# Kernel tuning notes

Hardware: AMD Instinct MI355X
Metric: run time of the kernel (lower is better)

Reference implementation:

```python
import jax, jax.numpy as jnp
import numpy as np

D_MODEL = 1024
NHEAD = 16
HEAD_DIM = D_MODEL // NHEAD
LN_EPS = 1e-5


def _layer_norm(x, g, b):
    mu = jnp.mean(x, axis=-1, keepdims=True)
    var = jnp.var(x, axis=-1, keepdims=True)
    return (x - mu) * jax.lax.rsqrt(var + LN_EPS) * g + b


def setup_inputs() -> dict:
    key = jax.random.key(0)
    ks = jax.random.split(key, 12)
    B, S = 2, 2048
    init = 0.02
    return {
        "query": jax.random.normal(ks[0], (B, S, D_MODEL), jnp.float32),
        "key_": jax.random.normal(ks[1], (B, S, D_MODEL), jnp.float32),
        "value": jax.random.normal(ks[2], (B, S, D_MODEL), jnp.float32),
        "Wq": jax.random.normal(ks[3], (D_MODEL, D_MODEL), jnp.float32) * init,
        "bq": jnp.zeros((D_MODEL,), jnp.float32),
        "Wk": jax.random.normal(ks[4], (D_MODEL, D_MODEL), jnp.float32) * init,
        "bk": jnp.zeros((D_MODEL,), jnp.float32),
        "Wv": jax.random.normal(ks[5], (D_MODEL, D_MODEL), jnp.float32) * init,
        "bv": jnp.zeros((D_MODEL,), jnp.float32),
        "Wo": jax.random.normal(ks[6], (D_MODEL, D_MODEL), jnp.float32) * init,
        "bo": jnp.zeros((D_MODEL,), jnp.float32),
        "ln_g": jnp.ones((D_MODEL,), jnp.float32),
        "ln_b": jnp.zeros((D_MODEL,), jnp.float32),
    }


def reference(query, key_, value, Wq, bq, Wk, bk, Wv, bv, Wo, bo, ln_g, ln_b):
    B, T, D = query.shape
    S = key_.shape[1]
    # shared LayerNorm applied to q, k, v inputs (as in the torch module)
    qn = _layer_norm(query, ln_g, ln_b)
    kn = _layer_norm(key_, ln_g, ln_b)
    vn = _layer_norm(value, ln_g, ln_b)
    # projections (torch Linear: x @ W.T + b)
    q = qn @ Wq.T + bq
    k = kn @ Wk.T + bk
    v = vn @ Wv.T + bv
    # [B, H, S, Dh]
    q = q.reshape(B, T, NHEAD, HEAD_DIM).transpose(0, 2, 1, 3)
    k = k.reshape(B, S, NHEAD, HEAD_DIM).transpose(0, 2, 1, 3)
    v = v.reshape(B, S, NHEAD, HEAD_DIM).transpose(0, 2, 1, 3)
    q = q * (HEAD_DIM ** -0.5)
    # [B, H, T, S] score matrix (explicitly materialized, as in source)
    scores = jnp.einsum("bhtd,bhsd->bhts", q, k)
    causal = jnp.triu(jnp.ones((T, S), dtype=bool), k=1)
    scores = jnp.where(causal, -jnp.inf, scores)
    attn = jax.nn.softmax(scores.astype(jnp.float32), axis=-1).astype(query.dtype)
    out = jnp.einsum("bhts,bhsd->bhtd", attn, v)
    out = out.transpose(0, 2, 1, 3).reshape(B, T, D)
    out = out @ Wo.T + bo
    return out, attn
```

## Files before the change

kernel.cpp:

```cpp
#include <hip/hip_runtime.h>
#include <hip/hip_bf16.h>

typedef unsigned short u16;
typedef unsigned int u32;
typedef __bf16 bf16x8 __attribute__((ext_vector_type(8)));
typedef float f32x4 __attribute__((ext_vector_type(4)));

__device__ __forceinline__ u16 f2bf(float f) {
  __hip_bfloat16 h = __float2bfloat16(f);
  u16 u;
  __builtin_memcpy(&u, &h, 2);
  return u;
}
__device__ __forceinline__ float bf2f(u16 u) {
  u32 b = ((u32)u) << 16;
  float f;
  __builtin_memcpy(&f, &b, 4);
  return f;
}

__device__ __forceinline__ void gload16(const u16* g, u16* l) {
  __builtin_amdgcn_global_load_lds(
      (const __attribute__((address_space(1))) u32*)g,
      (__attribute__((address_space(3))) u32*)l, 16, 0, 0);
}

__global__ __launch_bounds__(256) void ln_cast(
    const float* __restrict__ q, const float* __restrict__ k,
    const float* __restrict__ v, const float* __restrict__ g,
    const float* __restrict__ bb, u16* __restrict__ xn) {
  int row = blockIdx.x;
  int tsel = row >> 12;
  int r_in = row & 4095;
  const float* src = (tsel == 0) ? q : (tsel == 1) ? k : v;
  int tid = threadIdx.x;
  float4 x = ((const float4*)(src + (size_t)r_in * 1024))[tid];
  float s  = x.x + x.y + x.z + x.w;
  float ss = x.x * x.x + x.y * x.y + x.z * x.z + x.w * x.w;
  #pragma unroll
  for (int m = 1; m < 64; m <<= 1) { s += __shfl_xor(s, m); ss += __shfl_xor(ss, m); }
  __shared__ float red[8];
  int wid = tid >> 6;
  if ((tid & 63) == 0) { red[wid] = s; red[wid + 4] = ss; }
  __syncthreads();
  s  = red[0] + red[1] + red[2] + red[3];
  ss = red[4] + red[5] + red[6] + red[7];
  float mu  = s * (1.f / 1024.f);
  float var = ss * (1.f / 1024.f) - mu * mu;
  float rs  = rsqrtf(var + 1e-5f);
  float4 gv = ((const float4*)g)[tid];
  float4 bv = ((const float4*)bb)[tid];
  ushort4 o;
  o.x = f2bf((x.x - mu) * rs * gv.x + bv.x);
  o.y = f2bf((x.y - mu) * rs * gv.y + bv.y);
  o.z = f2bf((x.z - mu) * rs * gv.z + bv.z);
  o.w = f2bf((x.w - mu) * rs * gv.w + bv.w);
  ((ushort4*)(xn + (size_t)row * 1024))[tid] = o;
}

__global__ __launch_bounds__(256) void wcast(
    const float* __restrict__ wq, const float* __restrict__ wk,
    const float* __restrict__ wv, const float* __restrict__ wo,
    u16* __restrict__ dst) {
  int i = blockIdx.x * 256 + threadIdx.x;
  int e = i * 4;
  int sel = e >> 20;
  int loc = e & 1048575;
  const float* w = (sel == 0) ? wq : (sel == 1) ? wk : (sel == 2) ? wv : wo;
  float4 x = *(const float4*)(w + loc);
  ushort4 o;
  o.x = f2bf(x.x); o.y = f2bf(x.y); o.z = f2bf(x.z); o.w = f2bf(x.w);
  *(ushort4*)(dst + e) = o;
}

__global__ __launch_bounds__(256) void gemm_nt(
    const u16* __restrict__ A0, const u16* __restrict__ W0,
    const float* __restrict__ bias0, const float* __restrict__ bias1,
    const float* __restrict__ bias2,
    float* __restrict__ oF, u16* __restrict__ oP, u16* __restrict__ oVT,
    int mode) {
  __shared__ alignas(16) u16 Al[128][64];
  __shared__ alignas(16) u16 Bl[128][64];
  int z = blockIdx.z;
  const u16* A = A0 + (size_t)z * 4194304;
  const u16* W = W0 + (size_t)z * 1048576;
  const float* bias = (z == 0) ? bias0 : (z == 1) ? bias1 : bias2;
  int m0 = blockIdx.y * 128, n0 = blockIdx.x * 128;
  int tid = threadIdx.x;
  int lane = tid & 63, wid = tid >> 6;
  int wr = wid >> 1, wc = wid & 1;
  int l15 = lane & 15, lg = lane >> 4;
  int lr = lane >> 3, lc = lane & 7;

  f32x4 acc[4][4];
  #pragma unroll
  for (int i = 0; i < 4; ++i)
    #pragma unroll
    for (int j = 0; j < 4; ++j) acc[i][j] = (f32x4){0.f, 0.f, 0.f, 0.f};

  for (int kt = 0; kt < 1024; kt += 64) {
    __syncthreads();
    #pragma unroll
    for (int qq = 0; qq < 4; ++qq) {
      int rb = (qq * 4 + wid) * 8;
      gload16(A + (size_t)(m0 + rb + lr) * 1024 + kt + lc * 8, &Al[rb][0]);
      gload16(W + (size_t)(n0 + rb + lr) * 1024 + kt + lc * 8, &Bl[rb][0]);
    }
    __syncthreads();
    #pragma unroll
    for (int kb = 0; kb < 2; ++kb) {
      bf16x8 af[4], bw[4];
      #pragma unroll
      for (int i = 0; i < 4; ++i)
        af[i] = *(const bf16x8*)&Al[wr * 64 + i * 16 + l15][kb * 32 + lg * 8];
      #pragma unroll
      for (int j = 0; j < 4; ++j)
        bw[j] = *(const bf16x8*)&Bl[wc * 64 + j * 16 + l15][kb * 32 + lg * 8];
      #pragma unroll
      for (int i = 0; i < 4; ++i)
        #pragma unroll
        for (int j = 0; j < 4; ++j)
          acc[i][j] = __builtin_amdgcn_mfma_f32_16x16x32_bf16(af[i], bw[j], acc[i][j], 0, 0, 0);
    }
  }

  float scale = (mode == 1 && z == 0) ? 0.125f : 1.f;
  #pragma unroll
  for (int i = 0; i < 4; ++i) {
    #pragma unroll
    for (int j = 0; j < 4; ++j) {
      int n = n0 + wc * 64 + j * 16 + l15;
      float bn = bias[n];
      #pragma unroll
      for (int r = 0; r < 4; ++r) {
        int m = m0 + wr * 64 + i * 16 + lg * 4 + r;
        float val = (acc[i][j][r] + bn) * scale;
        if (mode == 0) {
          oF[(size_t)m * 1024 + n] = val;
        } else {
          int b = m >> 11, sIdx = m & 2047, h = n >> 6, d = n & 63;
          if (z == 2) {
            oVT[((size_t)((b * 16 + h) * 64 + d)) * 2048 + sIdx] = f2bf(val);
          } else {
            oP[(size_t)z * 4194304 +
               ((size_t)((b * 16 + h) * 2048 + sIdx)) * 64 + d] = f2bf(val);
          }
        }
      }
    }
  }
}

__global__ __launch_bounds__(256) void attn_kernel(
    const u16* __restrict__ proj, const u16* __restrict__ vt,
    float* __restrict__ attnOut, u16* __restrict__ oat) {
  __shared__ alignas(16) u16 Kl[64][64];
  __shared__ alignas(16) u16 Vt[64][64];
  __shared__ alignas(16) u16 Pl[4][16][72];
  const int t0 = blockIdx.x * 64;
  const int bh = blockIdx.y;
  const int tid = threadIdx.x;
  const int lane = tid & 63, w = tid >> 6;
  const int l15 = lane & 15, lg = lane >> 4;
  const int lr = lane >> 3, lc = lane & 7;
  const u16* Q = proj;
  const u16* K = proj + 4194304;
  const u16* VT = vt + (size_t)bh * 131072;

  float* attnB = attnOut + ((size_t)bh * 2048) * 2048;

  {
    const int zc0 = t0 + 64;
    const int rowLen = (2048 - zc0) >> 2;
    const float4 z4 = make_float4(0.f, 0.f, 0.f, 0.f);
    for (int r = w; r < 64; r += 4) {
      float4* rp = (float4*)(attnB + (size_t)(t0 + r) * 2048 + zc0);
      for (int cc = lane; cc < rowLen; cc += 64) rp[cc] = z4;
    }
  }

  bf16x8 qa[2];
  {
    size_t qoff = ((size_t)bh * 2048 + t0 + w * 16 + l15) * 64 + lg * 8;
    qa[0] = *(const bf16x8*)(Q + qoff);
    qa[1] = *(const bf16x8*)(Q + qoff + 32);
  }
  const int jmax = t0 >> 6;

  float lsum[4] = {0.f, 0.f, 0.f, 0.f};
  for (int j = 0; j <= jmax; ++j) {
    __syncthreads();
    #pragma unroll
    for (int qq = 0; qq < 2; ++qq) {
      int rb = (qq * 4 + w) * 8;
      gload16(K + ((size_t)bh * 2048 + j * 64 + rb + lr) * 64 + lc * 8, &Kl[rb][0]);
    }
    __syncthreads();
    #pragma unroll
    for (int c = 0; c < 4; ++c) {
      f32x4 s = {0.f, 0.f, 0.f, 0.f};
      #pragma unroll
      for (int kb = 0; kb < 2; ++kb) {
        bf16x8 bfr = *(const bf16x8*)&Kl[c * 16 + l15][kb * 32 + lg * 8];
        s = __builtin_amdgcn_mfma_f32_16x16x32_bf16(qa[kb], bfr, s, 0, 0, 0);
      }
      int col = j * 64 + c * 16 + l15;
      #pragma unroll
      for (int r = 0; r < 4; ++r) {
        int trow = t0 + w * 16 + lg * 4 + r;
        if (col <= trow) lsum[r] += __expf(s[r]);
      }
    }
  }
  #pragma unroll
  for (int r = 0; r < 4; ++r) {
    #pragma unroll
    for (int m = 1; m < 16; m <<= 1) lsum[r] += __shfl_xor(lsum[r], m);
    lsum[r] = 1.f / lsum[r];
  }

  f32x4 acc_o[4];
  #pragma unroll
  for (int c2 = 0; c2 < 4; ++c2) acc_o[c2] = (f32x4){0.f, 0.f, 0.f, 0.f};

  for (int j = 0; j <= jmax; ++j) {
    __syncthreads();
    #pragma unroll
    for (int qq = 0; qq < 2; ++qq) {
      int rb = (qq * 4 + w) * 8;
      gload16(K + ((size_t)bh * 2048 + j * 64 + rb + lr) * 64 + lc * 8, &Kl[rb][0]);
      gload16(VT + (size_t)(rb + lr) * 2048 + j * 64 + lc * 8, &Vt[rb][0]);
    }
    __syncthreads();
    #pragma unroll
    for (int c = 0; c < 4; ++c) {
      f32x4 s = {0.f, 0.f, 0.f, 0.f};
      #pragma unroll
      for (int kb = 0; kb < 2; ++kb) {
        bf16x8 bfr = *(const bf16x8*)&Kl[c * 16 + l15][kb * 32 + lg * 8];
        s = __builtin_amdgcn_mfma_f32_16x16x32_bf16(qa[kb], bfr, s, 0, 0, 0);
      }
      int col = j * 64 + c * 16 + l15;
      #pragma unroll
      for (int r = 0; r < 4; ++r) {
        int trow = t0 + w * 16 + lg * 4 + r;
        float av = (col <= trow) ? __expf(s[r]) * lsum[r] : 0.f;
        Pl[w][lg * 4 + r][c * 16 + l15] = f2bf(av);
      }
    }
    __syncthreads();
    #pragma unroll
    for (int rr = 0; rr < 4; ++rr) {
      int flat = rr * 256 + tid;
      int row = flat >> 4, c4 = flat & 15;
      ushort4 p4 = *(const ushort4*)&Pl[row >> 4][row & 15][c4 * 4];
      float4 f4;
      f4.x = bf2f(p4.x); f4.y = bf2f(p4.y); f4.z = bf2f(p4.z); f4.w = bf2f(p4.w);
      *(float4*)&attnB[(size_t)(t0 + row) * 2048 + j * 64 + c4 * 4] = f4;
    }
    #pragma unroll
    for (int kb = 0; kb < 2; ++kb) {
      bf16x8 pa = *(const bf16x8*)&Pl[w][l15][kb * 32 + lg * 8];
      #pragma unroll
      for (int c2 = 0; c2 < 4; ++c2) {
        bf16x8 bv = *(const bf16x8*)&Vt[c2 * 16 + l15][kb * 32 + lg * 8];
        acc_o[c2] = __builtin_amdgcn_mfma_f32_16x16x32_bf16(pa, bv, acc_o[c2], 0, 0, 0);
      }
    }
  }

  int b = bh >> 4, h = bh & 15;
  #pragma unroll
  for (int c2 = 0; c2 < 4; ++c2) {
    #pragma unroll
    for (int r = 0; r < 4; ++r) {
      int trow = t0 + w * 16 + lg * 4 + r;
      oat[((size_t)(b * 2048 + trow)) * 1024 + h * 64 + c2 * 16 + l15] =
          f2bf(acc_o[c2][r]);
    }
  }
}

extern "C" void kernel_launch(void* const* d_in, const int* in_sizes, int n_in,
                              void* d_out, int out_size, void* d_ws, size_t ws_size,
                              hipStream_t stream) {
  const float* q    = (const float*)d_in[0];
  const float* k    = (const float*)d_in[1];
  const float* v    = (const float*)d_in[2];
  const float* Wq   = (const float*)d_in[3];
  const float* bq   = (const float*)d_in[4];
  const float* Wk   = (const float*)d_in[5];
  const float* bk   = (const float*)d_in[6];
  const float* Wv   = (const float*)d_in[7];
  const float* bv   = (const float*)d_in[8];
  const float* Wo   = (const float*)d_in[9];
  const float* bo   = (const float*)d_in[10];
  const float* ln_g = (const float*)d_in[11];
  const float* ln_b = (const float*)d_in[12];

  u16* ws   = (u16*)d_ws;
  u16* xn   = ws;
  u16* wb   = ws + 12582912;
  u16* proj = ws + 16777216;
  u16* vt   = ws + 25165824;
  u16* oat  = ws + 29360128;
  float* out  = (float*)d_out;
  float* attn = out + 4194304;

  ln_cast<<<dim3(12288), dim3(256), 0, stream>>>(q, k, v, ln_g, ln_b, xn);
  wcast<<<dim3(4096), dim3(256), 0, stream>>>(Wq, Wk, Wv, Wo, wb);
  gemm_nt<<<dim3(8, 32, 3), dim3(256), 0, stream>>>(xn, wb, bq, bk, bv,
                                                    nullptr, proj, vt, 1);
  attn_kernel<<<dim3(32, 32), dim3(256), 0, stream>>>(proj, vt, attn, oat);
  gemm_nt<<<dim3(8, 32, 1), dim3(256), 0, stream>>>(oat, wb + 3 * 1048576, bo,
                                                    bo, bo, out, nullptr, nullptr, 0);
}
```

Before: 788.1 us.

## Drop softmax denominator pre-pass; write unnormalized probs then rescale separately

Removes the first QK^T pass that only computed row sums. The main loop now writes unnormalized exp scores to the attention output and to LDS for the PV matmul, and the normalization is applied at the end to the output accumulator. A separate rescale kernel re-reads and rewrites the causal half of the fp32 attention matrix using stored inverse sums. The QK MFMA operands are swapped so each lane holds four consecutive columns of one row, which allows direct float4 stores and drops the LDS round trip and one barrier. The cost is an extra read-modify-write pass over about 256MB of attention data, and P is fed to the PV matmul unnormalized in bf16.

After: 918.1 us. 16.5% more time.

```diff
diff --git a/kernel.cpp b/kernel.cpp
--- a/kernel.cpp
+++ b/kernel.cpp
@@ -11,12 +11,6 @@
   u16 u;
   __builtin_memcpy(&u, &h, 2);
   return u;
-}
-__device__ __forceinline__ float bf2f(u16 u) {
-  u32 b = ((u32)u) << 16;
-  float f;
-  __builtin_memcpy(&f, &b, 4);
-  return f;
 }
 
 __device__ __forceinline__ void gload16(const u16* g, u16* l) {
@@ -153,7 +147,8 @@
 
 __global__ __launch_bounds__(256) void attn_kernel(
     const u16* __restrict__ proj, const u16* __restrict__ vt,
-    float* __restrict__ attnOut, u16* __restrict__ oat) {
+    float* __restrict__ attnOut, u16* __restrict__ oat,
+    float* __restrict__ linvG) {
   __shared__ alignas(16) u16 Kl[64][64];
   __shared__ alignas(16) u16 Vt[64][64];
   __shared__ alignas(16) u16 Pl[4][16][72];
@@ -186,39 +181,9 @@
     qa[1] = *(const bf16x8*)(Q + qoff + 32);
   }
   const int jmax = t0 >> 6;
-
-  float lsum[4] = {0.f, 0.f, 0.f, 0.f};
-  for (int j = 0; j <= jmax; ++j) {
-    __syncthreads();
-    #pragma unroll
-    for (int qq = 0; qq < 2; ++qq) {
-      int rb = (qq * 4 + w) * 8;
-      gload16(K + ((size_t)bh * 2048 + j * 64 + rb + lr) * 64 + lc * 8, &Kl[rb][0]);
-    }
-    __syncthreads();
-    #pragma unroll
-    for (int c = 0; c < 4; ++c) {
-      f32x4 s = {0.f, 0.f, 0.f, 0.f};
-      #pragma unroll
-      for (int kb = 0; kb < 2; ++kb) {
-        bf16x8 bfr = *(const bf16x8*)&Kl[c * 16 + l15][kb * 32 + lg * 8];
-        s = __builtin_amdgcn_mfma_f32_16x16x32_bf16(qa[kb], bfr, s, 0, 0, 0);
-      }
-      int col = j * 64 + c * 16 + l15;
-      #pragma unroll
-      for (int r = 0; r < 4; ++r) {
-        int trow = t0 + w * 16 + lg * 4 + r;
-        if (col <= trow) lsum[r] += __expf(s[r]);
-      }
-    }
-  }
-  #pragma unroll
-  for (int r = 0; r < 4; ++r) {
-    #pragma unroll
-    for (int m = 1; m < 16; m <<= 1) lsum[r] += __shfl_xor(lsum[r], m);
-    lsum[r] = 1.f / lsum[r];
-  }
-
+  const int trow_qk = t0 + w * 16 + l15;
+
+  float lsum = 0.f;
   f32x4 acc_o[4];
   #pragma unroll
   for (int c2 = 0; c2 < 4; ++c2) acc_o[c2] = (f32x4){0.f, 0.f, 0.f, 0.f};
@@ -237,27 +202,24 @@
       f32x4 s = {0.f, 0.f, 0.f, 0.f};
       #pragma unroll
       for (int kb = 0; kb < 2; ++kb) {
-        bf16x8 bfr = *(const bf16x8*)&Kl[c * 16 + l15][kb * 32 + lg * 8];
-        s = __builtin_amdgcn_mfma_f32_16x16x32_bf16(qa[kb], bfr, s, 0, 0, 0);
+        bf16x8 ka = *(const bf16x8*)&Kl[c * 16 + l15][kb * 32 + lg * 8];
+        s = __builtin_amdgcn_mfma_f32_16x16x32_bf16(ka, qa[kb], s, 0, 0, 0);
       }
-      int col = j * 64 + c * 16 + l15;
+      int col0 = j * 64 + c * 16 + lg * 4;
+      float p[4];
       #pragma unroll
       for (int r = 0; r < 4; ++r) {
-        int trow = t0 + w * 16 + lg * 4 + r;
-        float av = (col <= trow) ? __expf(s[r]) * lsum[r] : 0.f;
-        Pl[w][lg * 4 + r][c * 16 + l15] = f2bf(av);
+        float e = __expf(s[r]);
+        p[r] = (col0 + r <= trow_qk) ? e : 0.f;
+        lsum += p[r];
       }
-    }
-    __syncthreads();
-    #pragma unroll
-    for (int rr = 0; rr < 4; ++rr) {
-      int flat = rr * 256 + tid;
-      int row = flat >> 4, c4 = flat & 15;
-      ushort4 p4 = *(const ushort4*)&Pl[row >> 4][row & 15][c4 * 4];
-      float4 f4;
-      f4.x = bf2f(p4.x); f4.y = bf2f(p4.y); f4.z = bf2f(p4.z); f4.w = bf2f(p4.w);
-      *(float4*)&attnB[(size_t)(t0 + row) * 2048 + j * 64 + c4 * 4] = f4;
-    }
+      *(float4*)&attnB[(size_t)trow_qk * 2048 + col0] =
+          make_float4(p[0], p[1], p[2], p[3]);
+      ushort4 pk;
+      pk.x = f2bf(p[0]); pk.y = f2bf(p[1]); pk.z = f2bf(p[2]); pk.w = f2bf(p[3]);
+      *(ushort4*)&Pl[w][l15][c * 16 + lg * 4] = pk;
+    }
+    __syncthreads();
     #pragma unroll
     for (int kb = 0; kb < 2; ++kb) {
       bf16x8 pa = *(const bf16x8*)&Pl[w][l15][kb * 32 + lg * 8];
@@ -269,6 +231,15 @@
     }
   }
 
+  lsum += __shfl_xor(lsum, 16);
+  lsum += __shfl_xor(lsum, 32);
+  float linv = 1.f / lsum;
+  if (lg == 0) linvG[(size_t)bh * 2048 + trow_qk] = linv;
+
+  float linv_r[4];
+  #pragma unroll
+  for (int r = 0; r < 4; ++r) linv_r[r] = __shfl(linv, lg * 4 + r);
+
   int b = bh >> 4, h = bh & 15;
   #pragma unroll
   for (int c2 = 0; c2 < 4; ++c2) {
@@ -276,7 +247,26 @@
     for (int r = 0; r < 4; ++r) {
       int trow = t0 + w * 16 + lg * 4 + r;
       oat[((size_t)(b * 2048 + trow)) * 1024 + h * 64 + c2 * 16 + l15] =
-          f2bf(acc_o[c2][r]);
+          f2bf(acc_o[c2][r] * linv_r[r]);
+    }
+  }
+}
+
+__global__ __launch_bounds__(256) void rescale_kernel(
+    float* __restrict__ attnOut, const float* __restrict__ linvG) {
+  const int t0 = blockIdx.x * 64;
+  const int bh = blockIdx.y;
+  const int tid = threadIdx.x;
+  const int lane = tid & 63, w = tid >> 6;
+  const int ncol4 = (t0 + 64) >> 2;
+  float* attnB = attnOut + ((size_t)bh * 2048) * 2048;
+  for (int r = w; r < 64; r += 4) {
+    float li = linvG[(size_t)bh * 2048 + t0 + r];
+    float4* rp = (float4*)(attnB + (size_t)(t0 + r) * 2048);
+    for (int cc = lane; cc < ncol4; cc += 64) {
+      float4 x = rp[cc];
+      x.x *= li; x.y *= li; x.z *= li; x.w *= li;
+      rp[cc] = x;
     }
   }
 }
@@ -304,6 +294,7 @@
   u16* proj = ws + 16777216;
   u16* vt   = ws + 25165824;
   u16* oat  = ws + 29360128;
+  float* linvG = (float*)(ws + 33554432);
   float* out  = (float*)d_out;
   float* attn = out + 4194304;
 
@@ -311,7 +302,8 @@
   wcast<<<dim3(4096), dim3(256), 0, stream>>>(Wq, Wk, Wv, Wo, wb);
   gemm_nt<<<dim3(8, 32, 3), dim3(256), 0, stream>>>(xn, wb, bq, bk, bv,
                                                     nullptr, proj, vt, 1);
-  attn_kernel<<<dim3(32, 32), dim3(256), 0, stream>>>(proj, vt, attn, oat);
+  attn_kernel<<<dim3(32, 32), dim3(256), 0, stream>>>(proj, vt, attn, oat, linvG);
+  rescale_kernel<<<dim3(32, 32), dim3(256), 0, stream>>>(attn, linvG);
   gemm_nt<<<dim3(8, 32, 1), dim3(256), 0, stream>>>(oat, wb + 3 * 1048576, bo,
                                                     bo, bo, out, nullptr, nullptr, 0);
 }
```
